# Kernel tuning notes

Measured on AMD Instinct MI355X. Metric: run time of the kernel, lower is better.

The kernel has to match this reference:

```python
import jax, jax.numpy as jnp
import numpy as np

B = 64                      # batch_size
MAX_STEPS = 100
FEAT = 6 + MAX_STEPS        # 106
REPEATS = 10
D = REPEATS * FEAT          # 1060
H = 256                     # policy_hidden_size
COUNTS = 32 * np.arange(B) + 16   # ragged segment sizes, sum=65536, max=2032
N = int(COUNTS.sum())
MAXLEN = int(COUNTS.max())
BN_EPS = 1e-5
LRELU_SLOPE = 0.01


def setup_inputs() -> dict:
    key = jax.random.key(0)
    k = jax.random.split(key, 6)
    seg = np.repeat(np.arange(B), COUNTS).astype(np.float32)  # column 0 = batch index
    features = jax.random.normal(k[0], (N, 1 + FEAT), jnp.float32)
    features = features.at[:, 0].set(jnp.asarray(seg))
    W1 = jax.random.normal(k[1], (D, H), jnp.float32) / np.sqrt(D)
    b1 = jax.random.normal(k[2], (H,), jnp.float32) * 0.01
    W2 = jax.random.normal(k[3], (H, 1), jnp.float32) / np.sqrt(H)
    b2 = jax.random.normal(k[4], (1,), jnp.float32) * 0.01
    return {
        "features": features,
        "bn_gamma": jnp.ones((D,), jnp.float32),
        "bn_beta": jnp.zeros((D,), jnp.float32),
        "W1": W1, "b1": b1, "W2": W2, "b2": b2,
        "max_len": MAXLEN,
    }


def reference(features, bn_gamma, bn_beta, W1, b1, W2, b2, max_len):
    seg = features[:, 0].astype(jnp.int32)                 # [N] batch indices
    x = jnp.tile(features[:, 1:], (1, REPEATS))            # [N, D] repeated features
    # BatchNorm1d (training mode: biased batch stats, as in the torch default)
    mean = jnp.mean(x, axis=0)
    var = jnp.var(x, axis=0)
    xn = (x - mean) * jax.lax.rsqrt(var + BN_EPS) * bn_gamma + bn_beta
    h = jnp.dot(xn, W1) + b1                               # [N, H]
    h = jnp.where(h >= 0, h, LRELU_SLOPE * h)              # LeakyReLU
    logits = (jnp.dot(h, W2) + b2)[:, 0]                   # [N]
    # segmented (ragged) log_softmax over each batch element's nodes
    m = jax.ops.segment_max(logits, seg, num_segments=B)   # [B]
    z = logits - m[seg]
    s = jax.ops.segment_sum(jnp.exp(z), seg, num_segments=B)
    logp = z - jnp.log(s)[seg]                             # [N]
    # scatter into padded [B, max_len] (-inf padding), position = rank within segment
    cnts = jax.ops.segment_sum(jnp.ones_like(seg), seg, num_segments=B)
    starts = jnp.cumsum(cnts) - cnts                       # exclusive prefix sum
    pos = jnp.arange(N, dtype=jnp.int32) - starts[seg]
    out = jnp.full((B, max_len), -jnp.inf, jnp.float32)
    return out.at[seg, pos].set(logp)
```

## Files before the change

### kernel.cpp

```cpp
#include <hip/hip_runtime.h>
#include <math.h>

#define NROWS   65536
#define NFEAT   106
#define NCOLIN  107
#define DREP    10
#define HID     256
#define BATCH   64
#define MAXLEN  2032
#define BN_EPS  1e-5f
#define SLOPE   0.01f
#define KPAD    128
#define NB_STATS 512
#define NEG_BIG (-1.0e30f)

#define WS_PART   0
#define WS_BACC   (WS_PART + NB_STATS*212)
#define WS_W1T    (WS_BACC + HID)
#define WS_FT     (WS_W1T + (HID*KPAD)/2)
#define WS_LOGITS (WS_FT + (NROWS*KPAD)/2)

typedef __attribute__((ext_vector_type(8))) short short8v;
typedef __attribute__((ext_vector_type(4))) float f32x4;

__device__ inline unsigned short f2bf(float x) {
    unsigned int u = __float_as_uint(x);
    return (unsigned short)((u + 0x7FFFu + ((u >> 16) & 1u)) >> 16);
}

__global__ __launch_bounds__(256) void k_stats(const float* __restrict__ feat,
                                               const float* __restrict__ b1,
                                               float* __restrict__ ws) {
    int tid  = threadIdx.x;
    int wave = tid >> 6, lane = tid & 63;
    int gw   = blockIdx.x * 4 + wave;
    if (blockIdx.x == 0) ws[WS_BACC + tid] = b1[tid];

    unsigned char* ft = (unsigned char*)(ws + WS_FT);
    int c0 = 2 * lane, c1 = 2 * lane + 1;
    bool act = (lane < 53);
    float s0 = 0.f, q0 = 0.f, s1 = 0.f, q1 = 0.f;
    for (int r = gw; r < NROWS; r += 2048) {
        const float* row = feat + (size_t)r * NCOLIN + 1;
        float v0 = 0.f, v1 = 0.f;
        if (act) { v0 = row[c0]; v1 = row[c1]; }
        s0 += v0; q0 += v0 * v0;
        s1 += v1; q1 += v1 * v1;
        unsigned int u = ((unsigned int)f2bf(v1) << 16) | f2bf(v0);
        *(unsigned int*)(ft + (size_t)r * 256 + lane * 4) = u;
    }
    __shared__ float red[4][64][4];
    red[wave][lane][0] = s0; red[wave][lane][1] = q0;
    red[wave][lane][2] = s1; red[wave][lane][3] = q1;
    __syncthreads();
    if (tid < 53) {
        float S0 = 0.f, Q0 = 0.f, S1 = 0.f, Q1 = 0.f;
        for (int w = 0; w < 4; ++w) {
            S0 += red[w][tid][0]; Q0 += red[w][tid][1];
            S1 += red[w][tid][2]; Q1 += red[w][tid][3];
        }
        float* p = ws + WS_PART + blockIdx.x * 212;
        p[2 * tid] = S0; p[2 * tid + 1] = S1;
        p[106 + 2 * tid] = Q0; p[107 + 2 * tid] = Q1;
    }
}

__global__ __launch_bounds__(256) void k_fold2(const float* __restrict__ gamma,
                                               const float* __restrict__ beta,
                                               const float* __restrict__ W1,
                                               float* __restrict__ ws) {
    int k = blockIdx.x;
    int j = threadIdx.x;
    unsigned char* w1t = (unsigned char*)(ws + WS_W1T);
    int byteW = j * 256 + 2 * k;
    if (k >= NFEAT) { *(unsigned short*)(w1t + byteW) = 0; return; }

    float S = ws[WS_PART + j * 212 + k]       + ws[WS_PART + (j + 256) * 212 + k];
    float Q = ws[WS_PART + j * 212 + 106 + k] + ws[WS_PART + (j + 256) * 212 + 106 + k];
    #pragma unroll
    for (int o = 32; o > 0; o >>= 1) { S += __shfl_xor(S, o); Q += __shfl_xor(Q, o); }
    __shared__ float r8[8];
    int w = j >> 6, l = j & 63;
    if (l == 0) { r8[w * 2] = S; r8[w * 2 + 1] = Q; }
    __syncthreads();
    S = r8[0] + r8[2] + r8[4] + r8[6];
    Q = r8[1] + r8[3] + r8[5] + r8[7];

    float mean = S * (1.0f / NROWS);
    float var  = Q * (1.0f / NROWS) - mean * mean;
    float rstd = rsqrtf(var + BN_EPS);

    float accW = 0.f, accB = 0.f;
    #pragma unroll
    for (int r = 0; r < DREP; ++r) {
        int d = r * NFEAT + k;
        float wv = W1[(size_t)d * HID + j];
        accW += gamma[d] * wv;
        accB += beta[d]  * wv;
    }
    float a = accW * rstd;
    *(unsigned short*)(w1t + byteW) = f2bf(a);
    atomicAdd(&ws[WS_BACC + j], accB - mean * a);
}

__global__ __launch_bounds__(256, 1) void k_mlp3(const float* __restrict__ W2,
                                                 const float* __restrict__ b2,
                                                 float* __restrict__ ws) {
    int tid = threadIdx.x;
    int w = tid >> 6, l = tid & 63;
    int lq = l >> 4, ln = l & 15;
    int gwid = blockIdx.x * 4 + w;

    const unsigned char* w1t = (const unsigned char*)(ws + WS_W1T);
    const unsigned char* ftb = (const unsigned char*)(ws + WS_FT);

    short8v bq[16][4];
    #pragma unroll
    for (int ct = 0; ct < 16; ++ct)
        #pragma unroll
        for (int ks = 0; ks < 4; ++ks)
            bq[ct][ks] = *(const short8v*)(w1t + (ct * 16 + ln) * 256 + ks * 64 + lq * 16);

    float b1r[16], w2r[16];
    #pragma unroll
    for (int ct = 0; ct < 16; ++ct) {
        b1r[ct] = ws[WS_BACC + ct * 16 + ln];
        w2r[ct] = W2[ct * 16 + ln];
    }
    float bias2 = b2[0];

    const unsigned char* abase = ftb + (size_t)gwid * 64 * 256;
    int aoff = ln * 256 + lq * 16;

    short8v a0[4], a1[4];
    #pragma unroll
    for (int ks = 0; ks < 4; ++ks)
        a0[ks] = *(const short8v*)(abase + aoff + ks * 64);

    #pragma unroll
    for (int t = 0; t < 4; ++t) {
        if (t < 3) {
            const unsigned char* an = abase + (t + 1) * 4096;
            #pragma unroll
            for (int ks = 0; ks < 4; ++ks)
                a1[ks] = *(const short8v*)(an + aoff + ks * 64);
        }
        float sp[4] = {0.f, 0.f, 0.f, 0.f};
        #pragma unroll
        for (int ct = 0; ct < 16; ++ct) {
            f32x4 acc = {b1r[ct], b1r[ct], b1r[ct], b1r[ct]};
            #pragma unroll
            for (int ks = 0; ks < 4; ++ks)
                acc = __builtin_amdgcn_mfma_f32_16x16x32_bf16(a0[ks], bq[ct][ks], acc, 0, 0, 0);
            #pragma unroll
            for (int reg = 0; reg < 4; ++reg) {
                float h = acc[reg];
                h = (h >= 0.f) ? h : SLOPE * h;
                sp[reg] += h * w2r[ct];
            }
        }
        #pragma unroll
        for (int reg = 0; reg < 4; ++reg) {
            float s = sp[reg];
            s += __shfl_xor(s, 1); s += __shfl_xor(s, 2);
            s += __shfl_xor(s, 4); s += __shfl_xor(s, 8);
            if (ln == 0)
                ws[WS_LOGITS + gwid * 64 + t * 16 + lq * 4 + reg] = s + bias2;
        }
        #pragma unroll
        for (int ks = 0; ks < 4; ++ks) a0[ks] = a1[ks];
    }
}

__global__ __launch_bounds__(256) void k_softmax(const float* __restrict__ ws,
                                                 float* __restrict__ out) {
    int b = blockIdx.x;
    int tid = threadIdx.x;
    int cnt = 32 * b + 16;
    int start = 16 * b * b;
    __shared__ float cache[MAXLEN];
    __shared__ float red[8];
    const float* lg = ws + WS_LOGITS + start;
    for (int i = tid; i < cnt; i += 256) cache[i] = lg[i];
    __syncthreads();

    float m = -1.0e30f;
    for (int i = tid; i < cnt; i += 256) m = fmaxf(m, cache[i]);
    #pragma unroll
    for (int o = 32; o > 0; o >>= 1) m = fmaxf(m, __shfl_xor(m, o));
    int wave = tid >> 6, lane = tid & 63;
    if (lane == 0) red[wave] = m;
    __syncthreads();
    m = fmaxf(fmaxf(red[0], red[1]), fmaxf(red[2], red[3]));

    float s = 0.f;
    for (int i = tid; i < cnt; i += 256) s += expf(cache[i] - m);
    #pragma unroll
    for (int o = 32; o > 0; o >>= 1) s += __shfl_xor(s, o);
    if (lane == 0) red[4 + wave] = s;
    __syncthreads();
    s = red[4] + red[5] + red[6] + red[7];
    float logC = m + logf(s);

    float* op = out + (size_t)b * MAXLEN;
    for (int i = tid; i < MAXLEN; i += 256)
        op[i] = (i < cnt) ? cache[i] - logC : NEG_BIG;
}

extern "C" void kernel_launch(void* const* d_in, const int* in_sizes, int n_in,
                              void* d_out, int out_size, void* d_ws, size_t ws_size,
                              hipStream_t stream) {
    const float* feat  = (const float*)d_in[0];
    const float* gamma = (const float*)d_in[1];
    const float* beta  = (const float*)d_in[2];
    const float* W1    = (const float*)d_in[3];
    const float* b1    = (const float*)d_in[4];
    const float* W2    = (const float*)d_in[5];
    const float* b2    = (const float*)d_in[6];
    float* ws  = (float*)d_ws;
    float* out = (float*)d_out;

    hipLaunchKernelGGL(k_stats,   dim3(NB_STATS), dim3(256), 0, stream, feat, b1, ws);
    hipLaunchKernelGGL(k_fold2,   dim3(KPAD),     dim3(256), 0, stream, gamma, beta, W1, ws);
    hipLaunchKernelGGL(k_mlp3,    dim3(256),      dim3(256), 0, stream, W2, b2, ws);
    hipLaunchKernelGGL(k_softmax, dim3(BATCH),    dim3(256), 0, stream, ws, out);
}
```

Before: 47.43 us.

## Stage folded W1 in swizzled LDS and spread MLP over more blocks

The MLP kernel no longer holds the whole bf16 W1 in per-lane registers. Each block now copies it into a 64KB LDS buffer with direct global-to-LDS loads, and the fold kernel writes it with an XOR swizzle so the LDS reads avoid bank conflicts. Each wave handles 32 rows instead of 64, and the grid doubles to 512 blocks, which cuts register pressure and should improve occupancy and latency hiding. In exchange, every block reloads W1 from L2, and the kernel pays an LDS read per column tile and a block barrier.

Measured after the change: 40.62 us. 1.17x faster.

```diff
diff --git a/kernel.cpp b/kernel.cpp
--- a/kernel.cpp
+++ b/kernel.cpp
@@ -28,6 +28,12 @@
     return (unsigned short)((u + 0x7FFFu + ((u >> 16) & 1u)) >> 16);
 }
 
+__device__ __forceinline__ void gload_lds16(const void* g, void* l) {
+    __builtin_amdgcn_global_load_lds(
+        (const __attribute__((address_space(1))) void*)(g),
+        (__attribute__((address_space(3))) void*)(l), 16, 0, 0);
+}
+
 __global__ __launch_bounds__(256) void k_stats(const float* __restrict__ feat,
                                                const float* __restrict__ b1,
                                                float* __restrict__ ws) {
@@ -72,7 +78,7 @@
     int k = blockIdx.x;
     int j = threadIdx.x;
     unsigned char* w1t = (unsigned char*)(ws + WS_W1T);
-    int byteW = j * 256 + 2 * k;
+    int byteW = j * 256 + ((2 * k) ^ ((j & 7) << 4));
     if (k >= NFEAT) { *(unsigned short*)(w1t + byteW) = 0; return; }
 
     float S = ws[WS_PART + j * 212 + k]       + ws[WS_PART + (j + 256) * 212 + k];
@@ -103,23 +109,27 @@
     atomicAdd(&ws[WS_BACC + j], accB - mean * a);
 }
 
-__global__ __launch_bounds__(256, 1) void k_mlp3(const float* __restrict__ W2,
-                                                 const float* __restrict__ b2,
-                                                 float* __restrict__ ws) {
+__global__ __launch_bounds__(256) void k_mlp4(const float* __restrict__ W2,
+                                              const float* __restrict__ b2,
+                                              float* __restrict__ ws) {
+    __shared__ __align__(16) unsigned char wl[65536];
     int tid = threadIdx.x;
     int w = tid >> 6, l = tid & 63;
     int lq = l >> 4, ln = l & 15;
-    int gwid = blockIdx.x * 4 + w;
-
-    const unsigned char* w1t = (const unsigned char*)(ws + WS_W1T);
-    const unsigned char* ftb = (const unsigned char*)(ws + WS_FT);
-
-    short8v bq[16][4];
-    #pragma unroll
-    for (int ct = 0; ct < 16; ++ct)
+
+    const unsigned char* wsrc = (const unsigned char*)(ws + WS_W1T);
+    #pragma unroll
+    for (int i = 0; i < 16; ++i)
+        gload_lds16(wsrc + (w * 16 + i) * 1024 + l * 16, wl + (w * 16 + i) * 1024);
+
+    int rowBase = blockIdx.x * 128 + w * 32;
+    const unsigned char* ab = (const unsigned char*)(ws + WS_FT) + (size_t)rowBase * 256;
+    short8v a[2][4];
+    #pragma unroll
+    for (int t = 0; t < 2; ++t)
         #pragma unroll
         for (int ks = 0; ks < 4; ++ks)
-            bq[ct][ks] = *(const short8v*)(w1t + (ct * 16 + ln) * 256 + ks * 64 + lq * 16);
+            a[t][ks] = *(const short8v*)(ab + t * 4096 + ln * 256 + ks * 64 + lq * 16);
 
     float b1r[16], w2r[16];
     #pragma unroll
@@ -128,48 +138,41 @@
         w2r[ct] = W2[ct * 16 + ln];
     }
     float bias2 = b2[0];
-
-    const unsigned char* abase = ftb + (size_t)gwid * 64 * 256;
-    int aoff = ln * 256 + lq * 16;
-
-    short8v a0[4], a1[4];
-    #pragma unroll
-    for (int ks = 0; ks < 4; ++ks)
-        a0[ks] = *(const short8v*)(abase + aoff + ks * 64);
-
-    #pragma unroll
-    for (int t = 0; t < 4; ++t) {
-        if (t < 3) {
-            const unsigned char* an = abase + (t + 1) * 4096;
-            #pragma unroll
-            for (int ks = 0; ks < 4; ++ks)
-                a1[ks] = *(const short8v*)(an + aoff + ks * 64);
-        }
-        float sp[4] = {0.f, 0.f, 0.f, 0.f};
-        #pragma unroll
-        for (int ct = 0; ct < 16; ++ct) {
+    __syncthreads();
+
+    float sp[2][4] = {{0.f,0.f,0.f,0.f},{0.f,0.f,0.f,0.f}};
+    #pragma unroll
+    for (int ct = 0; ct < 16; ++ct) {
+        int j = ct * 16 + ln;
+        int sw = (j & 7) << 4;
+        short8v bq[4];
+        #pragma unroll
+        for (int ks = 0; ks < 4; ++ks)
+            bq[ks] = *(const short8v*)(wl + j * 256 + ((ks * 64 + lq * 16) ^ sw));
+        #pragma unroll
+        for (int t = 0; t < 2; ++t) {
             f32x4 acc = {b1r[ct], b1r[ct], b1r[ct], b1r[ct]};
             #pragma unroll
             for (int ks = 0; ks < 4; ++ks)
-                acc = __builtin_amdgcn_mfma_f32_16x16x32_bf16(a0[ks], bq[ct][ks], acc, 0, 0, 0);
+                acc = __builtin_amdgcn_mfma_f32_16x16x32_bf16(a[t][ks], bq[ks], acc, 0, 0, 0);
             #pragma unroll
             for (int reg = 0; reg < 4; ++reg) {
                 float h = acc[reg];
                 h = (h >= 0.f) ? h : SLOPE * h;
-                sp[reg] += h * w2r[ct];
+                sp[t][reg] += h * w2r[ct];
             }
         }
+    }
+    #pragma unroll
+    for (int t = 0; t < 2; ++t)
         #pragma unroll
         for (int reg = 0; reg < 4; ++reg) {
-            float s = sp[reg];
+            float s = sp[t][reg];
             s += __shfl_xor(s, 1); s += __shfl_xor(s, 2);
             s += __shfl_xor(s, 4); s += __shfl_xor(s, 8);
             if (ln == 0)
-                ws[WS_LOGITS + gwid * 64 + t * 16 + lq * 4 + reg] = s + bias2;
+                ws[WS_LOGITS + rowBase + t * 16 + lq * 4 + reg] = s + bias2;
         }
-        #pragma unroll
-        for (int ks = 0; ks < 4; ++ks) a0[ks] = a1[ks];
-    }
 }
 
 __global__ __launch_bounds__(256) void k_softmax(const float* __restrict__ ws,
@@ -222,6 +225,6 @@
 
     hipLaunchKernelGGL(k_stats,   dim3(NB_STATS), dim3(256), 0, stream, feat, b1, ws);
     hipLaunchKernelGGL(k_fold2,   dim3(KPAD),     dim3(256), 0, stream, gamma, beta, W1, ws);
-    hipLaunchKernelGGL(k_mlp3,    dim3(256),      dim3(256), 0, stream, W2, b2, ws);
+    hipLaunchKernelGGL(k_mlp4,    dim3(512),      dim3(256), 0, stream, W2, b2, ws);
     hipLaunchKernelGGL(k_softmax, dim3(BATCH),    dim3(256), 0, stream, ws, out);
 }
```

## Fuse MLP with segmented softmax per batch segment; contiguous rows in stats

Applied to the files above, without the earlier changes.

Merges the MLP logits kernel and the segmented log-softmax kernel into one kernel with one block per batch segment. Logits stay in shared memory instead of making a global round trip, and one launch is removed. The stats kernel now gives each wave a contiguous run of rows with an unrolled loop, and the MLP loop issues all 16 column-tile MFMAs per k-step before the LeakyReLU/W2 reduction. The cost is only 64 blocks with ragged work: the largest segment has 127 tiles across 4 waves, so the critical path is much longer than with the previous 256 evenly loaded blocks.

Measured after the change: 92.40 us. 1.95x slower.

```diff
diff --git a/kernel.cpp b/kernel.cpp
--- a/kernel.cpp
+++ b/kernel.cpp
@@ -18,7 +18,6 @@
 #define WS_BACC   (WS_PART + NB_STATS*212)
 #define WS_W1T    (WS_BACC + HID)
 #define WS_FT     (WS_W1T + (HID*KPAD)/2)
-#define WS_LOGITS (WS_FT + (NROWS*KPAD)/2)
 
 typedef __attribute__((ext_vector_type(8))) short short8v;
 typedef __attribute__((ext_vector_type(4))) float f32x4;
@@ -33,14 +32,16 @@
                                                float* __restrict__ ws) {
     int tid  = threadIdx.x;
     int wave = tid >> 6, lane = tid & 63;
-    int gw   = blockIdx.x * 4 + wave;
     if (blockIdx.x == 0) ws[WS_BACC + tid] = b1[tid];
 
     unsigned char* ft = (unsigned char*)(ws + WS_FT);
-    int c0 = 2 * lane, c1 = 2 * lane + 1;
+    int c0 = 2 * lane, c1 = c0 + 1;
     bool act = (lane < 53);
+    int r0 = blockIdx.x * 128 + wave * 32;
     float s0 = 0.f, q0 = 0.f, s1 = 0.f, q1 = 0.f;
-    for (int r = gw; r < NROWS; r += 2048) {
+    #pragma unroll 4
+    for (int i = 0; i < 32; ++i) {
+        int r = r0 + i;
         const float* row = feat + (size_t)r * NCOLIN + 1;
         float v0 = 0.f, v1 = 0.f;
         if (act) { v0 = row[c0]; v1 = row[c1]; }
@@ -103,17 +104,21 @@
     atomicAdd(&ws[WS_BACC + j], accB - mean * a);
 }
 
-__global__ __launch_bounds__(256, 1) void k_mlp3(const float* __restrict__ W2,
-                                                 const float* __restrict__ b2,
-                                                 float* __restrict__ ws) {
+__global__ __launch_bounds__(256, 1) void k_mlpsm2(const float* __restrict__ W2,
+                                                   const float* __restrict__ b2,
+                                                   float* __restrict__ ws,
+                                                   float* __restrict__ out) {
+    __shared__ float cache[MAXLEN];
+    __shared__ float red[8];
     int tid = threadIdx.x;
     int w = tid >> 6, l = tid & 63;
     int lq = l >> 4, ln = l & 15;
-    int gwid = blockIdx.x * 4 + w;
+    int b = blockIdx.x;
+    int cnt = 32 * b + 16;
+    int start = 16 * b * b;
+    int ntiles = 2 * b + 1;
 
     const unsigned char* w1t = (const unsigned char*)(ws + WS_W1T);
-    const unsigned char* ftb = (const unsigned char*)(ws + WS_FT);
-
     short8v bq[16][4];
     #pragma unroll
     for (int ct = 0; ct < 16; ++ct)
@@ -129,67 +134,58 @@
     }
     float bias2 = b2[0];
 
-    const unsigned char* abase = ftb + (size_t)gwid * 64 * 256;
+    const unsigned char* ab = (const unsigned char*)(ws + WS_FT) + (size_t)start * 256;
     int aoff = ln * 256 + lq * 16;
 
-    short8v a0[4], a1[4];
-    #pragma unroll
-    for (int ks = 0; ks < 4; ++ks)
-        a0[ks] = *(const short8v*)(abase + aoff + ks * 64);
-
-    #pragma unroll
-    for (int t = 0; t < 4; ++t) {
-        if (t < 3) {
-            const unsigned char* an = abase + (t + 1) * 4096;
+    short8v acur[4], anxt[4];
+    if (w < ntiles) {
+        #pragma unroll
+        for (int ks = 0; ks < 4; ++ks)
+            acur[ks] = *(const short8v*)(ab + (size_t)w * 4096 + aoff + ks * 64);
+    }
+    for (int t = w; t < ntiles; t += 4) {
+        int tn = t + 4;
+        if (tn < ntiles) {
             #pragma unroll
             for (int ks = 0; ks < 4; ++ks)
-                a1[ks] = *(const short8v*)(an + aoff + ks * 64);
+                anxt[ks] = *(const short8v*)(ab + (size_t)tn * 4096 + aoff + ks * 64);
         }
+        f32x4 acc[16];
+        #pragma unroll
+        for (int ct = 0; ct < 16; ++ct)
+            acc[ct] = (f32x4){b1r[ct], b1r[ct], b1r[ct], b1r[ct]};
+        #pragma unroll
+        for (int ks = 0; ks < 4; ++ks)
+            #pragma unroll
+            for (int ct = 0; ct < 16; ++ct)
+                acc[ct] = __builtin_amdgcn_mfma_f32_16x16x32_bf16(acur[ks], bq[ct][ks], acc[ct], 0, 0, 0);
+
         float sp[4] = {0.f, 0.f, 0.f, 0.f};
         #pragma unroll
-        for (int ct = 0; ct < 16; ++ct) {
-            f32x4 acc = {b1r[ct], b1r[ct], b1r[ct], b1r[ct]};
-            #pragma unroll
-            for (int ks = 0; ks < 4; ++ks)
-                acc = __builtin_amdgcn_mfma_f32_16x16x32_bf16(a0[ks], bq[ct][ks], acc, 0, 0, 0);
+        for (int ct = 0; ct < 16; ++ct)
             #pragma unroll
             for (int reg = 0; reg < 4; ++reg) {
-                float h = acc[reg];
-                h = (h >= 0.f) ? h : SLOPE * h;
+                float h = acc[ct][reg];
+                h = fmaxf(h, SLOPE * h);
                 sp[reg] += h * w2r[ct];
             }
-        }
         #pragma unroll
         for (int reg = 0; reg < 4; ++reg) {
             float s = sp[reg];
             s += __shfl_xor(s, 1); s += __shfl_xor(s, 2);
             s += __shfl_xor(s, 4); s += __shfl_xor(s, 8);
-            if (ln == 0)
-                ws[WS_LOGITS + gwid * 64 + t * 16 + lq * 4 + reg] = s + bias2;
+            if (ln == 0) cache[t * 16 + lq * 4 + reg] = s + bias2;
         }
         #pragma unroll
-        for (int ks = 0; ks < 4; ++ks) a0[ks] = a1[ks];
-    }
-}
-
-__global__ __launch_bounds__(256) void k_softmax(const float* __restrict__ ws,
-                                                 float* __restrict__ out) {
-    int b = blockIdx.x;
-    int tid = threadIdx.x;
-    int cnt = 32 * b + 16;
-    int start = 16 * b * b;
-    __shared__ float cache[MAXLEN];
-    __shared__ float red[8];
-    const float* lg = ws + WS_LOGITS + start;
-    for (int i = tid; i < cnt; i += 256) cache[i] = lg[i];
+        for (int ks = 0; ks < 4; ++ks) acur[ks] = anxt[ks];
+    }
     __syncthreads();
 
     float m = -1.0e30f;
     for (int i = tid; i < cnt; i += 256) m = fmaxf(m, cache[i]);
     #pragma unroll
     for (int o = 32; o > 0; o >>= 1) m = fmaxf(m, __shfl_xor(m, o));
-    int wave = tid >> 6, lane = tid & 63;
-    if (lane == 0) red[wave] = m;
+    if (l == 0) red[w] = m;
     __syncthreads();
     m = fmaxf(fmaxf(red[0], red[1]), fmaxf(red[2], red[3]));
 
@@ -197,7 +193,7 @@
     for (int i = tid; i < cnt; i += 256) s += expf(cache[i] - m);
     #pragma unroll
     for (int o = 32; o > 0; o >>= 1) s += __shfl_xor(s, o);
-    if (lane == 0) red[4 + wave] = s;
+    if (l == 0) red[4 + w] = s;
     __syncthreads();
     s = red[4] + red[5] + red[6] + red[7];
     float logC = m + logf(s);
@@ -222,6 +218,5 @@
 
     hipLaunchKernelGGL(k_stats,   dim3(NB_STATS), dim3(256), 0, stream, feat, b1, ws);
     hipLaunchKernelGGL(k_fold2,   dim3(KPAD),     dim3(256), 0, stream, gamma, beta, W1, ws);
-    hipLaunchKernelGGL(k_mlp3,    dim3(256),      dim3(256), 0, stream, W2, b2, ws);
-    hipLaunchKernelGGL(k_softmax, dim3(BATCH),    dim3(256), 0, stream, ws, out);
-}
+    hipLaunchKernelGGL(k_mlpsm2,  dim3(BATCH),    dim3(256), 0, stream, W2, b2, ws, out);
+}
```
